# Performance work log

Hardware: AMD Instinct MI355X
Metric: run time of the kernel (lower is better)

## Reference

```python
import jax, jax.numpy as jnp
import numpy as np

NS, NA, T = 4, 4, 5
N = NS + NA
DT, TAU, SENS = 0.1, 0.25, 5.0
U_LO, U_HI = 0.0, 1.0
EPS, LQR_ITER = 0.01, 100


def build_problem(xd):
    """Replicates MPCLayer._init_model / _init_cost. xd: [B, NS]."""
    Bsz = xd.shape[0]
    A1 = jnp.array([[0, 0, 1, 0], [0, 0, 0, 1],
                    [0, 0, -TAU / DT, 0], [0, 0, 0, -TAU / DT]], jnp.float32)
    B1 = jnp.array([[0, 0, 0, 0], [0, 0, 0, 0],
                    [1, -1, 0, 0], [0, 0, 1, -1]], jnp.float32)
    Ad = jnp.eye(NS, dtype=jnp.float32) + A1 * DT
    Bd = B1 * DT * SENS
    Fm = jnp.tile(jnp.concatenate([Ad, Bd], axis=1)[None, None], (T, Bsz, 1, 1))  # [T,B,NS,N]
    w = jnp.array([1.0, 1.0, 0.1, 0.1], jnp.float32)
    q = jnp.concatenate([w, 0.1 * jnp.ones(NA, jnp.float32)])
    C = jnp.tile(jnp.diag(q)[None, None], (T, Bsz, 1, 1))  # [T,B,N,N]
    px = -jnp.sqrt(w) * xd  # [B,NS]
    p = jnp.concatenate([px, 0.01 * jnp.ones((Bsz, NA), jnp.float32)], axis=1)
    c = jnp.tile(p[None], (T, 1, 1))  # [T,B,N]
    return C, c, Fm


def rollout(x_init, u, Fm):
    """x_{t+1} = F_t [x_t; u_t]; returns states x_0..x_{T-1}: [T,B,NS]."""
    def step(x, tu):
        ut, Ft = tu
        x_next = jnp.einsum('bij,bj->bi', Ft, jnp.concatenate([x, ut], axis=-1))
        return x_next, x
    _, xs = jax.lax.scan(step, x_init, (u, Fm))
    return xs


def backward_pass(C, c_hat, Fm):
    """Riccati recursion; returns gains K:[T,B,NA,NS], k:[T,B,NA]."""
    Bsz = C.shape[1]

    def step(carry, inp):
        V, v = carry  # [B,NS,NS], [B,NS]
        Ct, ct, Ft = inp
        Qt = Ct + jnp.einsum('bxi,bxy,byj->bij', Ft, V, Ft)  # [B,N,N]
        qt = ct + jnp.einsum('bxi,bx->bi', Ft, v)            # [B,N]
        Qxx, Qxu = Qt[:, :NS, :NS], Qt[:, :NS, NS:]
        Qux, Quu = Qt[:, NS:, :NS], Qt[:, NS:, NS:]
        qx, qu = qt[:, :NS], qt[:, NS:]
        K = -jnp.linalg.solve(Quu, Qux)                       # [B,NA,NS]
        kk = -jnp.linalg.solve(Quu, qu[..., None])[..., 0]    # [B,NA]
        KtQuu = jnp.einsum('bui,buv->biv', K, Quu)
        V_new = Qxx + Qxu @ K + jnp.einsum('bui,buj->bij', K, Qux) + KtQuu @ K
        v_new = (qx + jnp.einsum('biu,bu->bi', Qxu, kk)
                 + jnp.einsum('bui,bu->bi', K, qu + jnp.einsum('buv,bv->bu', Quu, kk)))
        return (V_new, v_new), (K, kk)

    V0 = jnp.zeros((Bsz, NS, NS), jnp.float32)
    v0 = jnp.zeros((Bsz, NS), jnp.float32)
    _, (Ks, ks) = jax.lax.scan(step, (V0, v0), (C, c_hat, Fm), reverse=True)
    return Ks, ks


def lqr_iteration(u, x_init, C, c, Fm):
    """One box-constrained delta-LQR sweep around current control trajectory u."""
    xs = rollout(x_init, u, Fm)
    tau = jnp.concatenate([xs, u], axis=-1)                 # [T,B,N]
    c_hat = c + jnp.einsum('tbij,tbj->tbi', C, tau)         # cost gradient at tau
    Ks, ks = backward_pass(C, c_hat, Fm)

    def fstep(dx, inp):
        Kt, kt, ut, Ft = inp
        du = jnp.einsum('bui,bi->bu', Kt, dx) + kt
        u_new = jnp.clip(ut + du, U_LO, U_HI)
        dx_next = jnp.einsum('bij,bj->bi', Ft,
                             jnp.concatenate([dx, u_new - ut], axis=-1))
        return dx_next, u_new

    dx0 = jnp.zeros_like(x_init)
    _, u_new = jax.lax.scan(fstep, dx0, (Ks, ks, u, Fm))
    delta = jnp.max(jnp.abs(u_new - u))
    return u_new, delta


def setup_inputs() -> dict:
    key = jax.random.key(0)
    k1, k2 = jax.random.split(key)
    B = 65536
    x_init = jax.random.normal(k1, (B, NS), jnp.float32)
    xd = jax.random.normal(k2, (B, NS), jnp.float32)
    return {"x_init": x_init, "xd": xd}


def reference(x_init, xd):
    C, c, Fm = build_problem(xd)
    Bsz = xd.shape[0]
    u0 = jnp.zeros((T, Bsz, NA), jnp.float32)  # u_init=None -> zeros

    def cond(state):
        u, i, delta = state
        return (i < LQR_ITER) & (delta > EPS)

    def body(state):
        u, i, delta = state
        u_new, d = lqr_iteration(u, x_init, C, c, Fm)
        return (u_new, i + 1, d)

    u_fin, _, _ = jax.lax.while_loop(
        cond, body, (u0, jnp.int32(0), jnp.float32(jnp.inf)))
    return u_fin[0]  # nominal_actions[0]: [B, NA]
```

## Files before the change

### kernel.cpp

```cpp
#include <hip/hip_runtime.h>

#define T_HOR 5
#define MAXIT 100
#define KGRP  8
#define NGRP  ((MAXIT + KGRP - 1) / KGRP)
#define EPSC  0.01f

typedef float f2 __attribute__((ext_vector_type(2)));

__device__ __forceinline__ float iter_once(
    const float (&e_)[T_HOR], const float (&gp)[T_HOR], const float (&hp)[T_HOR],
    f2 pcp, f2 pcv,
    f2 (&xp)[T_HOR], f2 (&xv)[T_HOR],
    f2 (&ua)[T_HOR], f2 (&ub)[T_HOR])
{
    f2 uka[T_HOR], ukb[T_HOR];
    f2 vp = {0.f, 0.f}, vv = {0.f, 0.f};
    #pragma unroll
    for (int t = T_HOR-1; t >= 0; --t) {
        f2 du = ua[t] - ub[t];
        f2 D  = 0.1f*du + vv;
        f2 m  = e_[t]*D;
        f2 ka = (0.5f*du - m) - 0.1f;
        uka[t] = ka;
        ukb[t] = -ka - 0.2f;
        f2 qxp = (pcp + xp[t]) + vp;
        f2 qxv = (pcv + 0.1f*xv[t]) + 0.1f*vp + 0.75f*vv;
        vp = qxp - gp[t]*D;
        vv = qxv - hp[t]*D;
    }

    float dmax1 = 0.f, dmax2 = 0.f;
    f2 dp = {0.f, 0.f}, dv = {0.f, 0.f};
    #pragma unroll
    for (int t = 0; t < T_HOR; ++t) {
        f2 phi = gp[t]*dp + hp[t]*dv;
        f2 ra = uka[t] - phi;
        f2 rb = ukb[t] + phi;
        f2 na, nb;
        na.x = __builtin_amdgcn_fmed3f(ra.x, 0.f, 1.f);
        na.y = __builtin_amdgcn_fmed3f(ra.y, 0.f, 1.f);
        nb.x = __builtin_amdgcn_fmed3f(rb.x, 0.f, 1.f);
        nb.y = __builtin_amdgcn_fmed3f(rb.y, 0.f, 1.f);
        f2 dua = na - ua[t];
        f2 dub = nb - ub[t];
        dmax1 = fmaxf(dmax1, fmaxf(fabsf(dua.x), fabsf(dua.y)));
        dmax2 = fmaxf(dmax2, fmaxf(fabsf(dub.x), fabsf(dub.y)));
        xp[t] += dp; xv[t] += dv;
        f2 ndp = dp + 0.1f*dv;
        f2 ndv = 0.75f*dv + 0.5f*(dua - dub);
        dp = ndp; dv = ndv;
        ua[t] = na; ub[t] = nb;
    }
    return fmaxf(dmax1, dmax2);
}

__global__ __launch_bounds__(256)
void mpc_iter_kernel(const float4* __restrict__ x_init,
                     const float4* __restrict__ xd,
                     float4* __restrict__ out,
                     int* __restrict__ gmask,
                     int* __restrict__ cnt)
{
    const int b = blockIdx.x * 256 + threadIdx.x;

    const float4 xi  = x_init[b];
    const float4 xdv = xd[b];
    const float SQ01 = 0.31622776601683794f;
    f2 pcp = {-xdv.x, -xdv.y};
    f2 pcv = {-SQ01*xdv.z, -SQ01*xdv.w};

    float e_[T_HOR], gp[T_HOR], hp[T_HOR];
    {
        float Vpp = 0.f, Vpv = 0.f, Vvv = 0.f;
        #pragma unroll
        for (int t = T_HOR-1; t >= 0; --t) {
            float s  = 0.25f * Vvv;
            float tw = 0.1f + 2.f*s;
            float inv = 1.f / tw;
            e_[t] = 0.5f * inv;
            float g = 0.5f * Vpv;
            float h = 0.05f * Vpv + 0.375f * Vvv;
            gp[t] = g * inv;
            hp[t] = h * inv;
            float nVpp = 1.0f + Vpp - 2.f*g*gp[t];
            float nVpv = 0.1f*Vpp + 0.75f*Vpv - 2.f*g*hp[t];
            float nVvv = 0.1f + 0.01f*Vpp + 0.15f*Vpv + 0.5625f*Vvv - 2.f*h*hp[t];
            Vpp = nVpp; Vpv = nVpv; Vvv = nVvv;
        }
    }

    f2 z = {0.f, 0.f};
    f2 ua[T_HOR], ub[T_HOR], xp[T_HOR], xv[T_HOR];
    #pragma unroll
    for (int t = 0; t < T_HOR; ++t) { ua[t] = z; ub[t] = z; }
    xp[0] = f2{xi.x, xi.y};
    xv[0] = f2{xi.z, xi.w};
    #pragma unroll
    for (int t = 0; t < T_HOR-1; ++t) {
        xp[t+1] = xp[t] + 0.1f*xv[t];
        xv[t+1] = 0.75f*xv[t];
    }

    int it_base = 0;
    for (int g = 0; g < NGRP; ++g) {
        f2 cka[T_HOR], ckb[T_HOR], ckp[T_HOR], ckv[T_HOR];
        #pragma unroll
        for (int t = 0; t < T_HOR; ++t) {
            cka[t] = ua[t]; ckb[t] = ub[t]; ckp[t] = xp[t]; ckv[t] = xv[t];
        }

        const int gl = (MAXIT - it_base < KGRP) ? (MAXIT - it_base) : KGRP;
        unsigned mask = 0;
        for (int j = 0; j < gl; ++j) {
            float delta = iter_once(e_, gp, hp, pcp, pcv, xp, xv, ua, ub);
            mask |= (delta > EPSC ? 1u : 0u) << j;
        }

        int m = __syncthreads_or((int)mask);
        if (threadIdx.x == 0) {
            if (m) __hip_atomic_fetch_or(&gmask[g], m, __ATOMIC_RELEASE, __HIP_MEMORY_SCOPE_AGENT);
            __hip_atomic_fetch_add(&cnt[g], 1, __ATOMIC_ACQ_REL, __HIP_MEMORY_SCOPE_AGENT);
            while (__hip_atomic_load(&cnt[g], __ATOMIC_ACQUIRE, __HIP_MEMORY_SCOPE_AGENT) < (int)gridDim.x) {
                __builtin_amdgcn_s_sleep(2);
            }
        }
        __syncthreads();
        int gm = __hip_atomic_load(&gmask[g], __ATOMIC_ACQUIRE, __HIP_MEMORY_SCOPE_AGENT);

        int j0 = __ffs(~(unsigned)gm) - 1;
        if (j0 < gl) {
            #pragma unroll
            for (int t = 0; t < T_HOR; ++t) {
                ua[t] = cka[t]; ub[t] = ckb[t]; xp[t] = ckp[t]; xv[t] = ckv[t];
            }
            for (int j = 0; j <= j0; ++j) {
                iter_once(e_, gp, hp, pcp, pcv, xp, xv, ua, ub);
            }
            break;
        }
        it_base += KGRP;
        if (it_base >= MAXIT) break;
    }

    out[b] = make_float4(ua[0].x, ub[0].x, ua[0].y, ub[0].y);
}

extern "C" void kernel_launch(void* const* d_in, const int* in_sizes, int n_in,
                              void* d_out, int out_size, void* d_ws, size_t ws_size,
                              hipStream_t stream) {
    const float4* x_init = (const float4*)d_in[0];
    const float4* xd     = (const float4*)d_in[1];
    float4* out          = (float4*)d_out;
    int* gmask           = (int*)d_ws;
    int* cnt             = (int*)d_ws + NGRP;

    const int B = in_sizes[0] / 4;
    hipMemsetAsync(d_ws, 0, 2 * NGRP * sizeof(int), stream);

    dim3 grid(B / 256), block(256);
    mpc_iter_kernel<<<grid, block, 0, stream>>>(x_init, xd, out, gmask, cnt);
}
```

Measured before the change: 34.68 us.

## Split each batch element across two threads, one per decoupled axis

Each batch element's two independent axes (x/y position-velocity channels) now go to separate threads instead of being processed as float2 vectors in one thread. This doubles the thread count, which adds latency hiding and occupancy for the serial iteration chain, and the launch bounds now request two blocks per CU. The cost is twice as many blocks taking part in the grid-wide spin barrier, and strided loads from the float4 inputs. The output layout is preserved because interleaving the float2 writes gives the same (ua.x, ub.x, ua.y, ub.y) order.

```diff
diff --git a/kernel.cpp b/kernel.cpp
--- a/kernel.cpp
+++ b/kernel.cpp
@@ -6,77 +6,71 @@
 #define NGRP  ((MAXIT + KGRP - 1) / KGRP)
 #define EPSC  0.01f
 
-typedef float f2 __attribute__((ext_vector_type(2)));
-
 __device__ __forceinline__ float iter_once(
     const float (&e_)[T_HOR], const float (&gp)[T_HOR], const float (&hp)[T_HOR],
-    f2 pcp, f2 pcv,
-    f2 (&xp)[T_HOR], f2 (&xv)[T_HOR],
-    f2 (&ua)[T_HOR], f2 (&ub)[T_HOR])
+    float pc_p, float pc_v,
+    float (&xp)[T_HOR], float (&xv)[T_HOR],
+    float (&ua)[T_HOR], float (&ub)[T_HOR])
 {
-    f2 uka[T_HOR], ukb[T_HOR];
-    f2 vp = {0.f, 0.f}, vv = {0.f, 0.f};
+    float uka[T_HOR], ukb[T_HOR];
+    float vp = 0.f, vv = 0.f;
     #pragma unroll
     for (int t = T_HOR-1; t >= 0; --t) {
-        f2 du = ua[t] - ub[t];
-        f2 D  = 0.1f*du + vv;
-        f2 m  = e_[t]*D;
-        f2 ka = (0.5f*du - m) - 0.1f;
+        float du = ua[t] - ub[t];
+        float D  = 0.1f*du + vv;
+        float m  = e_[t]*D;
+        float ka = (0.5f*du - m) - 0.1f;
         uka[t] = ka;
         ukb[t] = -ka - 0.2f;
-        f2 qxp = (pcp + xp[t]) + vp;
-        f2 qxv = (pcv + 0.1f*xv[t]) + 0.1f*vp + 0.75f*vv;
+        float qxp = (pc_p + xp[t]) + vp;
+        float qxv = (pc_v + 0.1f*xv[t]) + 0.1f*vp + 0.75f*vv;
         vp = qxp - gp[t]*D;
         vv = qxv - hp[t]*D;
     }
 
-    float dmax1 = 0.f, dmax2 = 0.f;
-    f2 dp = {0.f, 0.f}, dv = {0.f, 0.f};
+    float dmaxa = 0.f, dmaxb = 0.f;
+    float dp = 0.f, dv = 0.f;
     #pragma unroll
     for (int t = 0; t < T_HOR; ++t) {
-        f2 phi = gp[t]*dp + hp[t]*dv;
-        f2 ra = uka[t] - phi;
-        f2 rb = ukb[t] + phi;
-        f2 na, nb;
-        na.x = __builtin_amdgcn_fmed3f(ra.x, 0.f, 1.f);
-        na.y = __builtin_amdgcn_fmed3f(ra.y, 0.f, 1.f);
-        nb.x = __builtin_amdgcn_fmed3f(rb.x, 0.f, 1.f);
-        nb.y = __builtin_amdgcn_fmed3f(rb.y, 0.f, 1.f);
-        f2 dua = na - ua[t];
-        f2 dub = nb - ub[t];
-        dmax1 = fmaxf(dmax1, fmaxf(fabsf(dua.x), fabsf(dua.y)));
-        dmax2 = fmaxf(dmax2, fmaxf(fabsf(dub.x), fabsf(dub.y)));
+        float phi = gp[t]*dp + hp[t]*dv;
+        float na = __builtin_amdgcn_fmed3f(uka[t] - phi, 0.f, 1.f);
+        float nb = __builtin_amdgcn_fmed3f(ukb[t] + phi, 0.f, 1.f);
+        float dua = na - ua[t], dub = nb - ub[t];
+        dmaxa = fmaxf(dmaxa, fabsf(dua));
+        dmaxb = fmaxf(dmaxb, fabsf(dub));
         xp[t] += dp; xv[t] += dv;
-        f2 ndp = dp + 0.1f*dv;
-        f2 ndv = 0.75f*dv + 0.5f*(dua - dub);
+        float ndp = dp + 0.1f*dv;
+        float ndv = 0.75f*dv + 0.5f*(dua - dub);
         dp = ndp; dv = ndv;
         ua[t] = na; ub[t] = nb;
     }
-    return fmaxf(dmax1, dmax2);
+    return fmaxf(dmaxa, dmaxb);
 }
 
-__global__ __launch_bounds__(256)
-void mpc_iter_kernel(const float4* __restrict__ x_init,
-                     const float4* __restrict__ xd,
-                     float4* __restrict__ out,
+__global__ __launch_bounds__(256, 2)
+void mpc_iter_kernel(const float* __restrict__ x_init,
+                     const float* __restrict__ xd,
+                     float2* __restrict__ out,
                      int* __restrict__ gmask,
                      int* __restrict__ cnt)
 {
-    const int b = blockIdx.x * 256 + threadIdx.x;
+    const int tid = blockIdx.x * 256 + threadIdx.x;
+    const int b = tid >> 1;
+    const int s = tid & 1;
 
-    const float4 xi  = x_init[b];
-    const float4 xdv = xd[b];
     const float SQ01 = 0.31622776601683794f;
-    f2 pcp = {-xdv.x, -xdv.y};
-    f2 pcv = {-SQ01*xdv.z, -SQ01*xdv.w};
+    const float xi_p = x_init[4*b + s];
+    const float xi_v = x_init[4*b + 2 + s];
+    const float pc_p = -xd[4*b + s];
+    const float pc_v = -SQ01 * xd[4*b + 2 + s];
 
     float e_[T_HOR], gp[T_HOR], hp[T_HOR];
     {
         float Vpp = 0.f, Vpv = 0.f, Vvv = 0.f;
         #pragma unroll
         for (int t = T_HOR-1; t >= 0; --t) {
-            float s  = 0.25f * Vvv;
-            float tw = 0.1f + 2.f*s;
+            float ss = 0.25f * Vvv;
+            float tw = 0.1f + 2.f*ss;
             float inv = 1.f / tw;
             e_[t] = 0.5f * inv;
             float g = 0.5f * Vpv;
@@ -90,12 +84,9 @@
         }
     }
 
-    f2 z = {0.f, 0.f};
-    f2 ua[T_HOR], ub[T_HOR], xp[T_HOR], xv[T_HOR];
-    #pragma unroll
-    for (int t = 0; t < T_HOR; ++t) { ua[t] = z; ub[t] = z; }
-    xp[0] = f2{xi.x, xi.y};
-    xv[0] = f2{xi.z, xi.w};
+    float ua[T_HOR] = {0,0,0,0,0}, ub[T_HOR] = {0,0,0,0,0};
+    float xp[T_HOR], xv[T_HOR];
+    xp[0] = xi_p; xv[0] = xi_v;
     #pragma unroll
     for (int t = 0; t < T_HOR-1; ++t) {
         xp[t+1] = xp[t] + 0.1f*xv[t];
@@ -104,7 +95,7 @@
 
     int it_base = 0;
     for (int g = 0; g < NGRP; ++g) {
-        f2 cka[T_HOR], ckb[T_HOR], ckp[T_HOR], ckv[T_HOR];
+        float cka[T_HOR], ckb[T_HOR], ckp[T_HOR], ckv[T_HOR];
         #pragma unroll
         for (int t = 0; t < T_HOR; ++t) {
             cka[t] = ua[t]; ckb[t] = ub[t]; ckp[t] = xp[t]; ckv[t] = xv[t];
@@ -113,7 +104,7 @@
         const int gl = (MAXIT - it_base < KGRP) ? (MAXIT - it_base) : KGRP;
         unsigned mask = 0;
         for (int j = 0; j < gl; ++j) {
-            float delta = iter_once(e_, gp, hp, pcp, pcv, xp, xv, ua, ub);
+            float delta = iter_once(e_, gp, hp, pc_p, pc_v, xp, xv, ua, ub);
             mask |= (delta > EPSC ? 1u : 0u) << j;
         }
 
@@ -135,7 +126,7 @@
                 ua[t] = cka[t]; ub[t] = ckb[t]; xp[t] = ckp[t]; xv[t] = ckv[t];
             }
             for (int j = 0; j <= j0; ++j) {
-                iter_once(e_, gp, hp, pcp, pcv, xp, xv, ua, ub);
+                iter_once(e_, gp, hp, pc_p, pc_v, xp, xv, ua, ub);
             }
             break;
         }
@@ -143,21 +134,22 @@
         if (it_base >= MAXIT) break;
     }
 
-    out[b] = make_float4(ua[0].x, ub[0].x, ua[0].y, ub[0].y);
+    out[tid] = make_float2(ua[0], ub[0]);
 }
 
 extern "C" void kernel_launch(void* const* d_in, const int* in_sizes, int n_in,
                               void* d_out, int out_size, void* d_ws, size_t ws_size,
                               hipStream_t stream) {
-    const float4* x_init = (const float4*)d_in[0];
-    const float4* xd     = (const float4*)d_in[1];
-    float4* out          = (float4*)d_out;
-    int* gmask           = (int*)d_ws;
-    int* cnt             = (int*)d_ws + NGRP;
+    const float* x_init = (const float*)d_in[0];
+    const float* xd     = (const float*)d_in[1];
+    float2* out         = (float2*)d_out;
+    int* gmask          = (int*)d_ws;
+    int* cnt            = (int*)d_ws + NGRP;
 
     const int B = in_sizes[0] / 4;
+    const int threads = 2 * B;
     hipMemsetAsync(d_ws, 0, 2 * NGRP * sizeof(int), stream);
 
-    dim3 grid(B / 256), block(256);
+    dim3 grid(threads / 256), block(256);
     mpc_iter_kernel<<<grid, block, 0, stream>>>(x_init, xd, out, gmask, cnt);
 }
```

New measurement: 49.95 us. 44.0% more time.
